# Optimization experiments

Hardware: AMD Instinct MI355X
Metric: run time of the kernel (lower is better)

The kernel has to match this reference:

```python
import jax, jax.numpy as jnp
import numpy as np

N_HEAD = 16

def setup_inputs() -> dict:
    key = jax.random.key(0)
    ks = jax.random.split(key, 6)
    C = 1024
    B, T, Tp = 8, 1024, 64
    s = 0.02
    return {
        "x": jax.random.normal(ks[0], (B, T, C), jnp.float32),
        "prefix_embd": jax.random.normal(ks[1], (B, Tp, C), jnp.float32),
        "w_attn": jax.random.normal(ks[2], (C, 3 * C), jnp.float32) * s,
        "b_attn": jnp.zeros((3 * C,), jnp.float32),
        "w_prefix": jax.random.normal(ks[3], (C, 3 * C), jnp.float32) * s,
        "b_prefix": jnp.zeros((3 * C,), jnp.float32),
        "w_proj": jax.random.normal(ks[4], (C, C), jnp.float32) * s,
        "b_proj": jnp.zeros((C,), jnp.float32),
    }

def _heads(t, H):
    B, T, C = t.shape
    return t.reshape(B, T, H, C // H).transpose(0, 2, 1, 3)  # (B,H,T,d)

def reference(x, prefix_embd, w_attn, b_attn, w_prefix, b_prefix, w_proj, b_proj):
    B, T, C = x.shape
    H = N_HEAD
    d = C // H
    Tp = prefix_embd.shape[1]
    scale = 1.0 / jnp.sqrt(jnp.asarray(d, x.dtype))

    qkv = x @ w_attn + b_attn
    q, k, v = (_heads(t, H) for t in jnp.split(qkv, 3, axis=2))  # (B,H,T,d)

    pqkv = prefix_embd @ w_prefix + b_prefix
    _, k_p, v_p = (_heads(t, H) for t in jnp.split(pqkv, 3, axis=2))  # (B,H,Tp,d)

    causal = jnp.tril(jnp.ones((T, T), bool))  # bias buffer slice
    neg_inf = jnp.asarray(float("-inf"), x.dtype)

    att = jnp.einsum("bhqd,bhkd->bhqk", q, k) * scale
    att = jnp.where(causal[None, None], att, neg_inf)
    att = jax.nn.softmax(att, axis=-1)

    att_p = jnp.einsum("bhqd,bhkd->bhqk", q, k_p) * scale
    att_p = jnp.where(causal[:, :Tp][None, None], att_p, neg_inf)
    att_p = jax.nn.softmax(att_p, axis=-1)

    y = jnp.einsum("bhqk,bhkd->bhqd", att_p, v_p) + jnp.einsum("bhqk,bhkd->bhqd", att, v)
    y = y.transpose(0, 2, 1, 3).reshape(B, T, C)
    return y @ w_proj + b_proj
```

## Files before the change

### kernel.cpp

```cpp
#include <hip/hip_runtime.h>
#include <hip/hip_bf16.h>
#include <cstdint>
#include <cstddef>

typedef __bf16 bf16_t;
typedef bf16_t bf16x8 __attribute__((ext_vector_type(8)));
typedef bf16_t bf16x4 __attribute__((ext_vector_type(4)));
typedef float f32x4 __attribute__((ext_vector_type(4)));

#define NB 8
#define NT 1024
#define NC 1024
#define NH 16
#define ND 64
#define NTP 64

__global__ __launch_bounds__(256) void k_cast2(const float* __restrict__ a, bf16_t* __restrict__ da,
                                               int n4a,
                                               const float* __restrict__ b2, bf16_t* __restrict__ db,
                                               int n4b) {
    int i = blockIdx.x * 256 + threadIdx.x;
    if (i < n4a) {
        float4 f = ((const float4*)a)[i];
        bf16x4 o;
        o[0] = (bf16_t)f.x; o[1] = (bf16_t)f.y; o[2] = (bf16_t)f.z; o[3] = (bf16_t)f.w;
        ((bf16x4*)da)[i] = o;
    } else {
        int j = i - n4a;
        if (j < n4b) {
            float4 f = ((const float4*)b2)[j];
            bf16x4 o;
            o[0] = (bf16_t)f.x; o[1] = (bf16_t)f.y; o[2] = (bf16_t)f.z; o[3] = (bf16_t)f.w;
            ((bf16x4*)db)[j] = o;
        }
    }
}

__global__ __launch_bounds__(256) void k_transpose3(const float* __restrict__ s0, bf16_t* __restrict__ d0,
                                                    const float* __restrict__ s1, bf16_t* __restrict__ d1,
                                                    const float* __restrict__ s2, bf16_t* __restrict__ d2) {
    __shared__ float tile[32][33];
    const int z = blockIdx.z;
    const float* src = (z == 0) ? s0 : (z == 1) ? s1 : s2;
    bf16_t* dst = (z == 0) ? d0 : (z == 1) ? d1 : d2;
    const int N = (z == 2) ? NC : 3 * NC;
    const int K = NC;
    if (z == 2 && blockIdx.x >= 32) return;
    int nt = blockIdx.x, kt = blockIdx.y;
    int tx = threadIdx.x & 31;
    int ty = threadIdx.x >> 5;
#pragma unroll
    for (int i = 0; i < 4; i++) {
        int r = ty + i * 8;
        tile[r][tx] = src[(size_t)(kt * 32 + r) * N + nt * 32 + tx];
    }
    __syncthreads();
#pragma unroll
    for (int i = 0; i < 4; i++) {
        int r = ty + i * 8;
        dst[(size_t)(nt * 32 + r) * K + kt * 32 + tx] = (bf16_t)tile[tx][r];
    }
}

template <int OMODE, int TSH>
__global__ __launch_bounds__(256) void k_gemm_f(const bf16_t* __restrict__ A,
                                                const bf16_t* __restrict__ BT,
                                                const float* __restrict__ bias,
                                                void* __restrict__ Cout,
                                                int M, int N, int K) {
    __shared__ bf16_t As[128 * 72];
    __shared__ bf16_t Bs[128 * 72];
    const int tid = threadIdx.x;
    const int lane = tid & 63;
    const int wave = tid >> 6;
    const int quad = lane >> 4;
    const int l15 = lane & 15;
    const int wm = (wave >> 1) * 64;
    const int wn = (wave & 1) * 64;
    const size_t rowA0 = (size_t)blockIdx.y * 128;
    const size_t colB0 = (size_t)blockIdx.x * 128;

    const f32x4 fz = {0.f, 0.f, 0.f, 0.f};
    f32x4 acc[4][4];
#pragma unroll
    for (int i = 0; i < 4; i++)
#pragma unroll
        for (int j = 0; j < 4; j++) acc[i][j] = fz;

    for (int k0 = 0; k0 < K; k0 += 64) {
        __syncthreads();
#pragma unroll
        for (int i = 0; i < 4; i++) {
            int c = tid + i * 256;
            int r = c >> 3;
            int kc = (c & 7) * 8;
            uint4 av = *(const uint4*)(A + (rowA0 + r) * (size_t)K + k0 + kc);
            *(uint4*)(&As[r * 72 + kc]) = av;
            uint4 bv = *(const uint4*)(BT + (colB0 + r) * (size_t)K + k0 + kc);
            *(uint4*)(&Bs[r * 72 + kc]) = bv;
        }
        __syncthreads();
#pragma unroll
        for (int kk = 0; kk < 2; kk++) {
            bf16x8 af[4], bfr[4];
#pragma unroll
            for (int i = 0; i < 4; i++)
                af[i] = *(const bf16x8*)(&As[(wm + i * 16 + l15) * 72 + kk * 32 + quad * 8]);
#pragma unroll
            for (int j = 0; j < 4; j++)
                bfr[j] = *(const bf16x8*)(&Bs[(wn + j * 16 + l15) * 72 + kk * 32 + quad * 8]);
#pragma unroll
            for (int i = 0; i < 4; i++)
#pragma unroll
                for (int j = 0; j < 4; j++)
                    acc[i][j] = __builtin_amdgcn_mfma_f32_16x16x32_bf16(af[i], bfr[j], acc[i][j], 0, 0, 0);
        }
    }
    const bool vpath = (OMODE == 2) && (colB0 >= (size_t)(2 * NC));
#pragma unroll
    for (int i = 0; i < 4; i++) {
        size_t row = rowA0 + wm + i * 16 + quad * 4;
#pragma unroll
        for (int j = 0; j < 4; j++) {
            int col = (int)colB0 + wn + j * 16 + l15;
            float bv = bias[col];
            if (vpath) {
                int hh = (col - 2 * NC) >> 6;
                int dd = col & 63;
                int bb = (int)(row >> TSH);
                int tt = (int)row & ((1 << TSH) - 1);
                int tileBase = (bb * NH + hh) * (1 << (TSH - 6)) + (tt >> 6);
                size_t chunkrow = (size_t)tileBase * 4 + (dd >> 4);
                size_t addr = chunkrow * (size_t)N + 2 * NC + (dd & 15) * 64 + (tt & 63);
                bf16x4 vv;
#pragma unroll
                for (int r = 0; r < 4; r++) vv[r] = (bf16_t)(acc[i][j][r] + bv);
                *(bf16x4*)((bf16_t*)Cout + addr) = vv;
            } else {
#pragma unroll
                for (int r = 0; r < 4; r++) {
                    float v = acc[i][j][r] + bv;
                    if (OMODE == 1)
                        ((float*)Cout)[(row + r) * (size_t)N + col] = v;
                    else
                        ((bf16_t*)Cout)[(row + r) * (size_t)N + col] = (bf16_t)v;
                }
            }
        }
    }
}


#define LOADREGS(KB, VCB)                                                            \
    rk0 = *(const uint4*)((KB) + (size_t)srow * 3072 + scol);                        \
    rk1 = *(const uint4*)((KB) + (size_t)(srow + 32) * 3072 + scol);                 \
    rv0 = *(const uint4*)((VCB) + (size_t)(tid >> 7) * 3072 + (tid & 127) * 8);      \
    rv1 = *(const uint4*)((VCB) + (size_t)((tid >> 7) + 2) * 3072 + (tid & 127) * 8);

#define STAGE(KS, VS)                                     \
    *(uint4*)(&(KS)[srow * 72 + scol]) = rk0;             \
    *(uint4*)(&(KS)[(srow + 32) * 72 + scol]) = rk1;      \
    *(uint4*)(&(VS)[srow * 72 + scol]) = rv0;             \
    *(uint4*)(&(VS)[(srow + 32) * 72 + scol]) = rv1;

#define QK(KS, Sj, j)                                                                  \
    Sj = __builtin_amdgcn_mfma_f32_16x16x32_bf16(                                      \
        aq0, *(const bf16x8*)(&(KS)[((j) * 16 + l15) * 72 + quad * 8]), Sj, 0, 0, 0);  \
    Sj = __builtin_amdgcn_mfma_f32_16x16x32_bf16(                                      \
        aq1, *(const bf16x8*)(&(KS)[((j) * 16 + l15) * 72 + 32 + quad * 8]), Sj, 0, 0, 0);

#define EXPJ(Sj, j, DIAG, LACC)                                         \
    {                                                                   \
        const int n_ = (j) * 16 + l15;                                  \
        _Pragma("unroll") for (int r_ = 0; r_ < 4; r_++) {              \
            float p_ = __expf(Sj[r_] * scale);                          \
            if ((DIAG) && n_ > wave * 16 + quad * 4 + r_) p_ = 0.f;     \
            Sj[r_] = p_;                                                \
            LACC[r_] += p_;                                             \
        }                                                               \
    }

#define PSTORE(Sj, j)                                                   \
    _Pragma("unroll") for (int r_ = 0; r_ < 4; r_++)                    \
        P[(quad * 4 + r_) * 72 + (j) * 16 + l15] = (bf16_t)Sj[r_];

#define PV(VS, Oj, j)                                                                  \
    Oj = __builtin_amdgcn_mfma_f32_16x16x32_bf16(                                      \
        ap0, *(const bf16x8*)(&(VS)[((j) * 16 + l15) * 72 + quad * 8]), Oj, 0, 0, 0);  \
    Oj = __builtin_amdgcn_mfma_f32_16x16x32_bf16(                                      \
        ap1, *(const bf16x8*)(&(VS)[((j) * 16 + l15) * 72 + 32 + quad * 8]), Oj, 0, 0, 0);

#define PROC(KS, VS, DIAG, LACC, O0, O1, O2, O3)                        \
    {                                                                   \
        f32x4 S0 = fz, S1 = fz, S2 = fz, S3 = fz;                       \
        __builtin_amdgcn_s_setprio(1);                                  \
        QK(KS, S0, 0) QK(KS, S1, 1) QK(KS, S2, 2) QK(KS, S3, 3)         \
        __builtin_amdgcn_s_setprio(0);                                  \
        EXPJ(S0, 0, DIAG, LACC) EXPJ(S1, 1, DIAG, LACC)                 \
        EXPJ(S2, 2, DIAG, LACC) EXPJ(S3, 3, DIAG, LACC)                 \
        PSTORE(S0, 0) PSTORE(S1, 1) PSTORE(S2, 2) PSTORE(S3, 3)         \
        __builtin_amdgcn_s_waitcnt(0xc07f);             \
        __builtin_amdgcn_wave_barrier();                                \
        bf16x8 ap0 = *(const bf16x8*)(&P[l15 * 72 + quad * 8]);         \
        bf16x8 ap1 = *(const bf16x8*)(&P[l15 * 72 + 32 + quad * 8]);    \
        __builtin_amdgcn_s_setprio(1);                                  \
        PV(VS, O0, 0) PV(VS, O1, 1) PV(VS, O2, 2) PV(VS, O3, 3)         \
        __builtin_amdgcn_s_setprio(0);                                  \
    }

#define STORE_O(Oj, Pj, j)                                                            \
    _Pragma("unroll") for (int r_ = 0; r_ < 4; r_++) {                                \
        float v_ = Oj[r_] * lmv[r_] + Pj[r_] * lpv[r_];                               \
        y[(qrow0 + quad * 4 + r_) * NC + h * 64 + (j) * 16 + l15] = (bf16_t)v_;       \
    }

__global__ __launch_bounds__(256, 2) void k_attn10(const bf16_t* __restrict__ qkv,
                                                   const bf16_t* __restrict__ pqkv,
                                                   bf16_t* __restrict__ y) {
    const int qt = (NT / 64 - 1) - blockIdx.x;
    const int h = blockIdx.y;
    const int b = blockIdx.z;

    __shared__ bf16_t Ks0[64 * 72], Ks1[64 * 72];
    __shared__ bf16_t Vs0[64 * 72], Vs1[64 * 72];
    __shared__ bf16_t Ps[4][16 * 72];

    const int tid = threadIdx.x;
    const int lane = tid & 63;
    const int wave = tid >> 6;
    const int quad = lane >> 4;
    const int l15 = lane & 15;
    const int srow = tid >> 3;
    const int scol = (tid & 7) * 8;
    const float scale = 0.125f;

    const size_t qrow0 = (size_t)b * NT + (size_t)qt * 64 + wave * 16;
    bf16_t* P = Ps[wave];

    const bf16_t* Kmain = qkv + (size_t)(b * NT) * 3072 + NC + h * 64;
    const bf16_t* Vmain = qkv + (size_t)(b * NH + h) * 16 * 4 * 3072 + 2 * NC;
    const bf16_t* Vpre  = pqkv + (size_t)(b * NH + h) * 4 * 3072 + 2 * NC;

    bf16x8 aq0 = *(const bf16x8*)(qkv + (qrow0 + l15) * 3072 + h * 64 + quad * 8);
    bf16x8 aq1 = *(const bf16x8*)(qkv + (qrow0 + l15) * 3072 + h * 64 + 32 + quad * 8);

    const f32x4 fz = {0.f, 0.f, 0.f, 0.f};
    f32x4 Om0 = fz, Om1 = fz, Om2 = fz, Om3 = fz;
    f32x4 Op0 = fz, Op1 = fz, Op2 = fz, Op3 = fz;
    f32x4 Lm = fz, Lp = fz;
    uint4 rk0, rk1, rv0, rv1;

    LOADREGS(pqkv + (size_t)(b * NTP) * 3072 + NC + h * 64, Vpre)
    STAGE(Ks0, Vs0)
    LOADREGS(Kmain, Vmain)
    __syncthreads();
    PROC(Ks0, Vs0, qt == 0, Lp, Op0, Op1, Op2, Op3)
    STAGE(Ks1, Vs1)
    if (qt >= 1) { LOADREGS(Kmain + (size_t)64 * 3072, Vmain + 4 * 3072) }

    for (int t = 0; t <= qt; t++) {
        __syncthreads();
        bf16_t* KSc = (t & 1) ? Ks0 : Ks1;
        bf16_t* VSc = (t & 1) ? Vs0 : Vs1;
        if (t < qt) {
            bf16_t* KSn = (t & 1) ? Ks1 : Ks0;
            bf16_t* VSn = (t & 1) ? Vs1 : Vs0;
            STAGE(KSn, VSn)
        }
        if (t + 1 < qt) {
            LOADREGS(Kmain + ((size_t)(t + 2) * 64) * 3072, Vmain + (size_t)(t + 2) * 4 * 3072)
        }
        PROC(KSc, VSc, t == qt, Lm, Om0, Om1, Om2, Om3)
    }

    f32x4 lmv, lpv;
#pragma unroll
    for (int r = 0; r < 4; r++) {
        float vm = Lm[r], vpr = Lp[r];
#pragma unroll
        for (int off = 1; off < 16; off <<= 1) {
            vm += __shfl_xor(vm, off, 64);
            vpr += __shfl_xor(vpr, off, 64);
        }
        lmv[r] = 1.0f / vm;
        lpv[r] = 1.0f / vpr;
    }

    STORE_O(Om0, Op0, 0) STORE_O(Om1, Op1, 1) STORE_O(Om2, Op2, 2) STORE_O(Om3, Op3, 3)
}

extern "C" void kernel_launch(void* const* d_in, const int* in_sizes, int n_in,
                              void* d_out, int out_size, void* d_ws, size_t ws_size,
                              hipStream_t stream) {
    (void)in_sizes; (void)n_in; (void)out_size; (void)ws_size;
    const float* x        = (const float*)d_in[0];
    const float* prefix   = (const float*)d_in[1];
    const float* w_attn   = (const float*)d_in[2];
    const float* b_attn   = (const float*)d_in[3];
    const float* w_prefix = (const float*)d_in[4];
    const float* b_prefix = (const float*)d_in[5];
    const float* w_proj   = (const float*)d_in[6];
    const float* b_proj   = (const float*)d_in[7];
    float* out = (float*)d_out;

    char* p = (char*)d_ws;
    auto carve = [&](size_t bytes) {
        char* q = p;
        p += (bytes + 255) & ~(size_t)255;
        return q;
    };
    bf16_t* xb   = (bf16_t*)carve((size_t)NB * NT * NC * 2);
    bf16_t* pb   = (bf16_t*)carve((size_t)NB * NTP * NC * 2);
    bf16_t* wTa  = (bf16_t*)carve((size_t)3 * NC * NC * 2);
    bf16_t* wTp  = (bf16_t*)carve((size_t)3 * NC * NC * 2);
    bf16_t* wTpr = (bf16_t*)carve((size_t)NC * NC * 2);
    bf16_t* qkv  = (bf16_t*)carve((size_t)NB * NT * 3 * NC * 2);
    bf16_t* pqkv = (bf16_t*)carve((size_t)NB * NTP * 3 * NC * 2);
    bf16_t* yb   = (bf16_t*)carve((size_t)NB * NT * NC * 2);

    const int n4a = NB * NT * NC / 4, n4b = NB * NTP * NC / 4;
    k_cast2<<<(n4a + n4b + 255) / 256, 256, 0, stream>>>(x, xb, n4a, prefix, pb, n4b);
    k_transpose3<<<dim3(3 * NC / 32, NC / 32, 3), 256, 0, stream>>>(w_attn, wTa, w_prefix, wTp,
                                                                    w_proj, wTpr);
    k_gemm_f<2, 10><<<dim3(3 * NC / 128, NB * NT / 128), 256, 0, stream>>>(
        xb, wTa, b_attn, qkv, NB * NT, 3 * NC, NC);
    k_gemm_f<2, 6><<<dim3(3 * NC / 128, NB * NTP / 128), 256, 0, stream>>>(
        pb, wTp, b_prefix, pqkv, NB * NTP, 3 * NC, NC);
    k_attn10<<<dim3(NT / 64, NH, NB), 256, 0, stream>>>(qkv, pqkv, yb);
    k_gemm_f<1, 6><<<dim3(NC / 128, NB * NT / 128), 256, 0, stream>>>(
        yb, wTpr, b_proj, out, NB * NT, NC, NC);
}
```

Before: 310.9 us.

## Widen attention query tile to 128 rows with 8 waves sharing K/V tiles

The attention kernel now processes 128 query rows per block with 512 threads (8 waves), so each staged 64-row K/V tile in shared memory serves twice as many queries. Each thread loads one K and one V vector per tile instead of two. The causal mask becomes a per-element offset comparison applied on every tile, not only the diagonal one. The aim is to halve global K/V traffic and staging per query. In exchange there are half as many blocks, a larger block, per-element mask compares on all tiles, and wasted work on the last masked tile for the lower waves.

```diff
diff --git a/kernel.cpp b/kernel.cpp
--- a/kernel.cpp
+++ b/kernel.cpp
@@ -152,16 +152,12 @@
 
 
 #define LOADREGS(KB, VCB)                                                            \
-    rk0 = *(const uint4*)((KB) + (size_t)srow * 3072 + scol);                        \
-    rk1 = *(const uint4*)((KB) + (size_t)(srow + 32) * 3072 + scol);                 \
-    rv0 = *(const uint4*)((VCB) + (size_t)(tid >> 7) * 3072 + (tid & 127) * 8);      \
-    rv1 = *(const uint4*)((VCB) + (size_t)((tid >> 7) + 2) * 3072 + (tid & 127) * 8);
-
-#define STAGE(KS, VS)                                     \
-    *(uint4*)(&(KS)[srow * 72 + scol]) = rk0;             \
-    *(uint4*)(&(KS)[(srow + 32) * 72 + scol]) = rk1;      \
-    *(uint4*)(&(VS)[srow * 72 + scol]) = rv0;             \
-    *(uint4*)(&(VS)[(srow + 32) * 72 + scol]) = rv1;
+    rk0 = *(const uint4*)((KB) + (size_t)(tid >> 3) * 3072 + (tid & 7) * 8);         \
+    rv0 = *(const uint4*)((VCB) + (size_t)(tid >> 7) * 3072 + (tid & 127) * 8);
+
+#define STAGE(KS, VS)                                                \
+    *(uint4*)(&(KS)[(tid >> 3) * 72 + (tid & 7) * 8]) = rk0;         \
+    *(uint4*)(&(VS)[(tid >> 3) * 72 + (tid & 7) * 8]) = rv0;
 
 #define QK(KS, Sj, j)                                                                  \
     Sj = __builtin_amdgcn_mfma_f32_16x16x32_bf16(                                      \
@@ -169,12 +165,12 @@
     Sj = __builtin_amdgcn_mfma_f32_16x16x32_bf16(                                      \
         aq1, *(const bf16x8*)(&(KS)[((j) * 16 + l15) * 72 + 32 + quad * 8]), Sj, 0, 0, 0);
 
-#define EXPJ(Sj, j, DIAG, LACC)                                         \
+#define EXPJ(Sj, j, BL, LACC)                                           \
     {                                                                   \
         const int n_ = (j) * 16 + l15;                                  \
         _Pragma("unroll") for (int r_ = 0; r_ < 4; r_++) {              \
             float p_ = __expf(Sj[r_] * scale);                          \
-            if ((DIAG) && n_ > wave * 16 + quad * 4 + r_) p_ = 0.f;     \
+            if (n_ > (BL) + r_) p_ = 0.f;                               \
             Sj[r_] = p_;                                                \
             LACC[r_] += p_;                                             \
         }                                                               \
@@ -190,14 +186,14 @@
     Oj = __builtin_amdgcn_mfma_f32_16x16x32_bf16(                                      \
         ap1, *(const bf16x8*)(&(VS)[((j) * 16 + l15) * 72 + 32 + quad * 8]), Oj, 0, 0, 0);
 
-#define PROC(KS, VS, DIAG, LACC, O0, O1, O2, O3)                        \
+#define PROC(KS, VS, BL, LACC, O0, O1, O2, O3)                          \
     {                                                                   \
         f32x4 S0 = fz, S1 = fz, S2 = fz, S3 = fz;                       \
         __builtin_amdgcn_s_setprio(1);                                  \
         QK(KS, S0, 0) QK(KS, S1, 1) QK(KS, S2, 2) QK(KS, S3, 3)         \
         __builtin_amdgcn_s_setprio(0);                                  \
-        EXPJ(S0, 0, DIAG, LACC) EXPJ(S1, 1, DIAG, LACC)                 \
-        EXPJ(S2, 2, DIAG, LACC) EXPJ(S3, 3, DIAG, LACC)                 \
+        EXPJ(S0, 0, BL, LACC) EXPJ(S1, 1, BL, LACC)                     \
+        EXPJ(S2, 2, BL, LACC) EXPJ(S3, 3, BL, LACC)                     \
         PSTORE(S0, 0) PSTORE(S1, 1) PSTORE(S2, 2) PSTORE(S3, 3)         \
         __builtin_amdgcn_s_waitcnt(0xc07f);             \
         __builtin_amdgcn_wave_barrier();                                \
@@ -214,27 +210,27 @@
         y[(qrow0 + quad * 4 + r_) * NC + h * 64 + (j) * 16 + l15] = (bf16_t)v_;       \
     }
 
-__global__ __launch_bounds__(256, 2) void k_attn10(const bf16_t* __restrict__ qkv,
+__global__ __launch_bounds__(512, 2) void k_attn11(const bf16_t* __restrict__ qkv,
                                                    const bf16_t* __restrict__ pqkv,
                                                    bf16_t* __restrict__ y) {
-    const int qt = (NT / 64 - 1) - blockIdx.x;
+    const int qt = (NT / 128 - 1) - blockIdx.x;
     const int h = blockIdx.y;
     const int b = blockIdx.z;
+    const int TMAX = 2 * qt + 1;
 
     __shared__ bf16_t Ks0[64 * 72], Ks1[64 * 72];
     __shared__ bf16_t Vs0[64 * 72], Vs1[64 * 72];
-    __shared__ bf16_t Ps[4][16 * 72];
+    __shared__ bf16_t Ps[8][16 * 72];
 
     const int tid = threadIdx.x;
     const int lane = tid & 63;
     const int wave = tid >> 6;
     const int quad = lane >> 4;
     const int l15 = lane & 15;
-    const int srow = tid >> 3;
-    const int scol = (tid & 7) * 8;
     const float scale = 0.125f;
 
-    const size_t qrow0 = (size_t)b * NT + (size_t)qt * 64 + wave * 16;
+    const size_t qrow0 = (size_t)b * NT + (size_t)qt * 128 + wave * 16;
+    const int qoff = qt * 128 + wave * 16 + quad * 4;
     bf16_t* P = Ps[wave];
 
     const bf16_t* Kmain = qkv + (size_t)(b * NT) * 3072 + NC + h * 64;
@@ -248,29 +244,29 @@
     f32x4 Om0 = fz, Om1 = fz, Om2 = fz, Om3 = fz;
     f32x4 Op0 = fz, Op1 = fz, Op2 = fz, Op3 = fz;
     f32x4 Lm = fz, Lp = fz;
-    uint4 rk0, rk1, rv0, rv1;
+    uint4 rk0, rv0;
 
     LOADREGS(pqkv + (size_t)(b * NTP) * 3072 + NC + h * 64, Vpre)
     STAGE(Ks0, Vs0)
     LOADREGS(Kmain, Vmain)
     __syncthreads();
-    PROC(Ks0, Vs0, qt == 0, Lp, Op0, Op1, Op2, Op3)
+    PROC(Ks0, Vs0, qoff, Lp, Op0, Op1, Op2, Op3)
     STAGE(Ks1, Vs1)
-    if (qt >= 1) { LOADREGS(Kmain + (size_t)64 * 3072, Vmain + 4 * 3072) }
-
-    for (int t = 0; t <= qt; t++) {
+    LOADREGS(Kmain + (size_t)64 * 3072, Vmain + 4 * 3072)
+
+    for (int t = 0; t <= TMAX; t++) {
         __syncthreads();
         bf16_t* KSc = (t & 1) ? Ks0 : Ks1;
         bf16_t* VSc = (t & 1) ? Vs0 : Vs1;
-        if (t < qt) {
+        if (t < TMAX) {
             bf16_t* KSn = (t & 1) ? Ks1 : Ks0;
             bf16_t* VSn = (t & 1) ? Vs1 : Vs0;
             STAGE(KSn, VSn)
         }
-        if (t + 1 < qt) {
+        if (t + 1 < TMAX) {
             LOADREGS(Kmain + ((size_t)(t + 2) * 64) * 3072, Vmain + (size_t)(t + 2) * 4 * 3072)
         }
-        PROC(KSc, VSc, t == qt, Lm, Om0, Om1, Om2, Om3)
+        PROC(KSc, VSc, qoff - t * 64, Lm, Om0, Om1, Om2, Om3)
     }
 
     f32x4 lmv, lpv;
@@ -326,7 +322,7 @@
         xb, wTa, b_attn, qkv, NB * NT, 3 * NC, NC);
     k_gemm_f<2, 6><<<dim3(3 * NC / 128, NB * NTP / 128), 256, 0, stream>>>(
         pb, wTp, b_prefix, pqkv, NB * NTP, 3 * NC, NC);
-    k_attn10<<<dim3(NT / 64, NH, NB), 256, 0, stream>>>(qkv, pqkv, yb);
+    k_attn11<<<dim3(NT / 128, NH, NB), 512, 0, stream>>>(qkv, pqkv, yb);
     k_gemm_f<1, 6><<<dim3(NC / 128, NB * NT / 128), 256, 0, stream>>>(
         yb, wTpr, b_proj, out, NB * NT, NC, NC);
 }
```

New measurement: 307.9 us. Within noise of the previous version (-1.0%).
